# Optimization experiments

Hardware: AMD Instinct MI355X
Metric: run time of the kernel (lower is better)

## Reference

```python
import jax, jax.numpy as jnp
import numpy as np

N_NODES = 50000
N_EDGES = 800000
IN_DIM, HID_DIM, OUT_DIM = 128, 128, 64


def setup_inputs() -> dict:
    key = jax.random.key(0)
    ks = jax.random.split(key, 12)
    x = jax.random.normal(ks[0], (N_NODES, IN_DIM), dtype=jnp.float32)
    src = jax.random.randint(ks[1], (N_EDGES,), 0, N_NODES, dtype=jnp.int32)
    dst = jax.random.randint(ks[2], (N_EDGES,), 0, N_NODES, dtype=jnp.int32)
    def lin(k, fan_in, fan_out):
        s = 1.0 / np.sqrt(fan_in)
        kw, kb = jax.random.split(k)
        W = jax.random.uniform(kw, (fan_in, fan_out), jnp.float32, -s, s)
        b = jax.random.uniform(kb, (fan_out,), jnp.float32, -s, s)
        return W, b
    W1, b1 = lin(ks[3], IN_DIM, HID_DIM)
    W2, b2 = lin(ks[4], HID_DIM, HID_DIM)
    W3, b3 = lin(ks[5], HID_DIM, OUT_DIM)
    Wf, bf = lin(ks[6], OUT_DIM, 1)
    return {"x": x, "src": src, "dst": dst,
            "W1": W1, "b1": b1, "W2": W2, "b2": b2,
            "W3": W3, "b3": b3, "Wf": Wf, "bf": bf}


def reference(x, src, dst, W1, b1, W2, b2, W3, b3, Wf, bf):
    n = x.shape[0]
    # GCN symmetric norm with self-loops: deg = in-degree + 1 (self loop)
    ones = jnp.ones(src.shape[0], x.dtype)
    deg = jax.ops.segment_sum(ones, dst, num_segments=n) + 1.0
    dinv = jax.lax.rsqrt(deg)                       # [N]
    edge_norm = dinv[src] * dinv[dst]               # [E]
    self_norm = dinv * dinv                         # [N], self-loop weight

    def gcn(h, W, b):
        h = h @ W                                   # transform first (PyG order)
        agg = jax.ops.segment_sum(h[src] * edge_norm[:, None], dst, num_segments=n)
        agg = agg + h * self_norm[:, None]          # self-loop contribution
        return agg + b

    h = jax.nn.relu(gcn(x, W1, b1))
    h = jax.nn.relu(gcn(h, W2, b2))
    h = jax.nn.relu(gcn(h, W3, b3))
    return h @ Wf + bf                              # [N, 1] per-node scores
```

## Files before the change

### kernel.cpp

```cpp
#include <hip/hip_runtime.h>
#include <hip/hip_bf16.h>

typedef short bf16x8 __attribute__((ext_vector_type(8)));
typedef float f32x4 __attribute__((ext_vector_type(4)));
typedef _Float16 f16x2 __attribute__((ext_vector_type(2)));

static __device__ __forceinline__ unsigned short f2bf_rne(float f) {
    unsigned int u = __float_as_uint(f);
    u += 0x7fff + ((u >> 16) & 1);
    return (unsigned short)(u >> 16);
}
static __device__ __forceinline__ float bf2f(unsigned short h) {
    return __uint_as_float(((unsigned int)h) << 16);
}

static __device__ __forceinline__ void wsplit_one(const float* W, unsigned short* hi,
                                                  unsigned short* lo, int BN, int idx) {
    int k = idx / BN, n = idx % BN;
    float w = W[idx];
    unsigned short h = f2bf_rne(w);
    unsigned short l = f2bf_rne(w - bf2f(h));
    int CT = BN >> 4;
    int kc = k >> 5, quad = (k >> 3) & 3, j = k & 7;
    int ct = n >> 4, c = n & 15;
    int slot = (((kc * CT + ct) * 4 + quad) * 16 + c) * 8 + j;
    hi[slot] = h;
    lo[slot] = l;
}


template<int BN>
static __device__ __forceinline__ void gemm_body(const float* __restrict__ A,
                        const unsigned short* __restrict__ Whi, const unsigned short* __restrict__ Wlo,
                        _Float16* __restrict__ C, int N, int blk,
                        unsigned short* AhiS, unsigned short* AloS) {
    constexpr int CT = BN / 16;
    const int tid = threadIdx.x;
    const int wave = tid >> 6;
    const int lane = tid & 63;
    const int quad = lane >> 4;
    const int c16 = lane & 15;
    const int row0 = blk * 64;

    f32x4 acc[CT];
    #pragma unroll
    for (int t = 0; t < CT; ++t) acc[t] = (f32x4){0.f, 0.f, 0.f, 0.f};

    for (int kc = 0; kc < 4; ++kc) {
        #pragma unroll
        for (int r = 0; r < 2; ++r) {
            int f4 = tid + r * 256;
            int arow = f4 >> 3;
            int c4 = f4 & 7;
            int grow = row0 + arow;
            float4 v = make_float4(0.f, 0.f, 0.f, 0.f);
            if (grow < N) v = *(const float4*)&A[(size_t)grow * 128 + kc * 32 + c4 * 4];
            unsigned short h0 = f2bf_rne(v.x), h1 = f2bf_rne(v.y), h2 = f2bf_rne(v.z), h3 = f2bf_rne(v.w);
            ushort4 hv = make_ushort4(h0, h1, h2, h3);
            ushort4 lv = make_ushort4(f2bf_rne(v.x - bf2f(h0)), f2bf_rne(v.y - bf2f(h1)),
                                      f2bf_rne(v.z - bf2f(h2)), f2bf_rne(v.w - bf2f(h3)));
            int q = c4 >> 1;
            int joff = (c4 & 1) * 4;
            int base = (q * 64 + arow) * 8 + joff;
            *(ushort4*)&AhiS[base] = hv;
            *(ushort4*)&AloS[base] = lv;
        }
        __syncthreads();

        int abase = (quad * 64 + wave * 16 + c16) * 8;
        bf16x8 ahi = *(const bf16x8*)&AhiS[abase];
        bf16x8 alo = *(const bf16x8*)&AloS[abase];

        #pragma unroll
        for (int ct = 0; ct < CT; ++ct) {
            size_t bslot = ((size_t)(kc * CT + ct) * 64 + lane) * 8;
            bf16x8 bhi = *(const bf16x8*)&Whi[bslot];
            bf16x8 blo = *(const bf16x8*)&Wlo[bslot];
            acc[ct] = __builtin_amdgcn_mfma_f32_16x16x32_bf16(ahi, bhi, acc[ct], 0, 0, 0);
            acc[ct] = __builtin_amdgcn_mfma_f32_16x16x32_bf16(ahi, blo, acc[ct], 0, 0, 0);
            acc[ct] = __builtin_amdgcn_mfma_f32_16x16x32_bf16(alo, bhi, acc[ct], 0, 0, 0);
        }
        __syncthreads();
    }

    #pragma unroll
    for (int ct = 0; ct < CT; ++ct) {
        int col = ct * 16 + c16;
        _Float16* Cq = C + (size_t)(col >> 5) * N * 32 + (col & 31);
        #pragma unroll
        for (int r = 0; r < 4; ++r) {
            int grow = row0 + wave * 16 + quad * 4 + r;
            if (grow < N) Cq[(size_t)grow * 32] = (_Float16)acc[ct][r];
        }
    }
}


__global__ __launch_bounds__(256) void k_count_wsplit(const int* __restrict__ dst, int* __restrict__ deg,
                          int* __restrict__ rank,
                          const float* __restrict__ W1, const float* __restrict__ W2, const float* __restrict__ W3,
                          unsigned short* __restrict__ W1hi, unsigned short* __restrict__ W1lo,
                          unsigned short* __restrict__ W2hi, unsigned short* __restrict__ W2lo,
                          unsigned short* __restrict__ W3hi, unsigned short* __restrict__ W3lo,
                          int E) {
    int e = blockIdx.x * blockDim.x + threadIdx.x;
    if (e < E) rank[e] = atomicAdd(&deg[dst[e]], 1);
    if (e < 128 * 128) {
        wsplit_one(W1, W1hi, W1lo, 128, e);
        wsplit_one(W2, W2hi, W2lo, 128, e);
    }
    if (e < 128 * 64) wsplit_one(W3, W3hi, W3lo, 64, e);
}

__global__ __launch_bounds__(1024) void k_scan(const int* __restrict__ deg, float* __restrict__ dinv,
                                               int* __restrict__ row_start,
                                               float* __restrict__ outp, const float* __restrict__ bf,
                                               int N) {
    __shared__ int s[1024];
    __shared__ int wsum[16];
    __shared__ int prefix;
    const int t = threadIdx.x;
    const int base = blockIdx.x * 1024;

    {
        int v = 0;
        for (int j = t; j < base; j += 1024) v += deg[j];
        for (int off = 32; off > 0; off >>= 1) v += __shfl_down(v, off, 64);
        if ((t & 63) == 0) wsum[t >> 6] = v;
        __syncthreads();
        if (t == 0) {
            int acc = 0;
            #pragma unroll
            for (int k = 0; k < 16; ++k) acc += wsum[k];
            prefix = acc;
        }
    }

    int i = base + t;
    int v = 0;
    if (i < N) {
        v = deg[i];
        dinv[i] = rsqrtf((float)v + 1.0f);
        outp[i] = bf[0];
    }
    s[t] = v;
    __syncthreads();
    for (int off = 1; off < 1024; off <<= 1) {
        int x = (t >= off) ? s[t - off] : 0;
        __syncthreads();
        s[t] += x;
        __syncthreads();
    }
    if (i <= N) row_start[i] = prefix + s[t] - v;
}


__global__ __launch_bounds__(256, 2) void k_gemm1_scatter(const float* __restrict__ A,
                          const unsigned short* __restrict__ Whi, const unsigned short* __restrict__ Wlo,
                          _Float16* __restrict__ C, int N, int gemmGrid,
                          const int* __restrict__ src, const int* __restrict__ dst,
                          const int* __restrict__ row_start, const int* __restrict__ rank,
                          const float* __restrict__ dinv, int2* __restrict__ cv, int E) {
    __shared__ unsigned short AhiS[4 * 64 * 8];
    __shared__ unsigned short AloS[4 * 64 * 8];
    if ((int)blockIdx.x < gemmGrid) {
        gemm_body<128>(A, Whi, Wlo, C, N, blockIdx.x, AhiS, AloS);
    } else {
        int e = (blockIdx.x - gemmGrid) * 256 + threadIdx.x;
        if (e < E) {
            int d = dst[e];
            int s = src[e];
            cv[row_start[d] + rank[e]] = make_int2(s, __float_as_int(dinv[s]));
        }
    }
}

template<int BN>
__global__ __launch_bounds__(256, 2) void k_gemm_mfma(const float* __restrict__ A,
                        const unsigned short* __restrict__ Whi, const unsigned short* __restrict__ Wlo,
                        _Float16* __restrict__ C, int N) {
    __shared__ unsigned short AhiS[4 * 64 * 8];
    __shared__ unsigned short AloS[4 * 64 * 8];
    gemm_body<BN>(A, Whi, Wlo, C, N, blockIdx.x, AhiS, AloS);
}


__global__ __launch_bounds__(256) void k_agg128q(const _Float16* __restrict__ t, float* __restrict__ outp,
                      const int* __restrict__ row_start, const int2* __restrict__ cv,
                      const float* __restrict__ dinv, const float* __restrict__ bias,
                      int N) {
    int q = blockIdx.x / 12500;
    int node = (blockIdx.x - q * 12500) * 4 + (threadIdx.x >> 6);
    int lane = threadIdx.x & 63;
    int l16 = lane & 15;
    int g4 = lane >> 4;
    const f16x2* tp = (const f16x2*)(t + (size_t)q * N * 32);
    int p = row_start[node];
    int end = row_start[node + 1];
    float2 accA = make_float2(0.f, 0.f);
    float2 accB = make_float2(0.f, 0.f);

    while (p < end) {
        int idx = p + lane;
        int2 h = (idx < end) ? cv[idx] : make_int2(0, 0);
        int cnt = min(end - p, 64);
        int rounds = (cnt + 15) >> 4;
        for (int r = 0; r < rounds; ++r) {
            int base = r * 16 + g4 * 4;
            int s0 = __shfl(h.x, base + 0, 64), s1 = __shfl(h.x, base + 1, 64);
            int s2 = __shfl(h.x, base + 2, 64), s3 = __shfl(h.x, base + 3, 64);
            float w0 = __int_as_float(__shfl(h.y, base + 0, 64));
            float w1 = __int_as_float(__shfl(h.y, base + 1, 64));
            float w2 = __int_as_float(__shfl(h.y, base + 2, 64));
            float w3 = __int_as_float(__shfl(h.y, base + 3, 64));
            f16x2 v0 = tp[s0 * 16 + l16];
            f16x2 v1 = tp[s1 * 16 + l16];
            f16x2 v2 = tp[s2 * 16 + l16];
            f16x2 v3 = tp[s3 * 16 + l16];
            accA.x += w0 * (float)v0.x; accA.y += w0 * (float)v0.y;
            accB.x += w1 * (float)v1.x; accB.y += w1 * (float)v1.y;
            accA.x += w2 * (float)v2.x; accA.y += w2 * (float)v2.y;
            accB.x += w3 * (float)v3.x; accB.y += w3 * (float)v3.y;
        }
        p += 64;
    }
    float sx = accA.x + accB.x;
    float sy = accA.y + accB.y;
    sx += __shfl_xor(sx, 16, 64); sx += __shfl_xor(sx, 32, 64);
    sy += __shfl_xor(sy, 16, 64); sy += __shfl_xor(sy, 32, 64);

    float di = dinv[node];
    f16x2 sv = tp[node * 16 + l16];
    float2 bv = ((const float2*)bias)[q * 16 + l16];
    float rx = fmaxf(di * sx + di * di * (float)sv.x + bv.x, 0.f);
    float ry = fmaxf(di * sy + di * di * (float)sv.y + bv.y, 0.f);
    if (lane < 16)
        ((float2*)outp)[(size_t)node * 64 + q * 16 + l16] = make_float2(rx, ry);
}

__global__ __launch_bounds__(256) void k_agg64_final(const _Float16* __restrict__ t, float* __restrict__ outp,
                      const int* __restrict__ row_start, const int2* __restrict__ cv,
                      const float* __restrict__ dinv, const float* __restrict__ bias,
                      const float* __restrict__ Wf,
                      int N) {
    int q = blockIdx.x / 12500;
    int node = (blockIdx.x - q * 12500) * 4 + (threadIdx.x >> 6);
    int lane = threadIdx.x & 63;
    int l16 = lane & 15;
    int g4 = lane >> 4;
    const f16x2* tp = (const f16x2*)(t + (size_t)q * N * 32);
    int p = row_start[node];
    int end = row_start[node + 1];
    float2 accA = make_float2(0.f, 0.f);
    float2 accB = make_float2(0.f, 0.f);

    while (p < end) {
        int idx = p + lane;
        int2 h = (idx < end) ? cv[idx] : make_int2(0, 0);
        int cnt = min(end - p, 64);
        int rounds = (cnt + 15) >> 4;
        for (int r = 0; r < rounds; ++r) {
            int base = r * 16 + g4 * 4;
            int s0 = __shfl(h.x, base + 0, 64), s1 = __shfl(h.x, base + 1, 64);
            int s2 = __shfl(h.x, base + 2, 64), s3 = __shfl(h.x, base + 3, 64);
            float w0 = __int_as_float(__shfl(h.y, base + 0, 64));
            float w1 = __int_as_float(__shfl(h.y, base + 1, 64));
            float w2 = __int_as_float(__shfl(h.y, base + 2, 64));
            float w3 = __int_as_float(__shfl(h.y, base + 3, 64));
            f16x2 v0 = tp[s0 * 16 + l16];
            f16x2 v1 = tp[s1 * 16 + l16];
            f16x2 v2 = tp[s2 * 16 + l16];
            f16x2 v3 = tp[s3 * 16 + l16];
            accA.x += w0 * (float)v0.x; accA.y += w0 * (float)v0.y;
            accB.x += w1 * (float)v1.x; accB.y += w1 * (float)v1.y;
            accA.x += w2 * (float)v2.x; accA.y += w2 * (float)v2.y;
            accB.x += w3 * (float)v3.x; accB.y += w3 * (float)v3.y;
        }
        p += 64;
    }
    float sx = accA.x + accB.x;
    float sy = accA.y + accB.y;
    sx += __shfl_xor(sx, 16, 64); sx += __shfl_xor(sx, 32, 64);
    sy += __shfl_xor(sy, 16, 64); sy += __shfl_xor(sy, 32, 64);

    float di = dinv[node];
    f16x2 sv = tp[node * 16 + l16];
    float2 bv = ((const float2*)bias)[q * 16 + l16];
    float rx = fmaxf(di * sx + di * di * (float)sv.x + bv.x, 0.f);
    float ry = fmaxf(di * sy + di * di * (float)sv.y + bv.y, 0.f);
    float2 wf = ((const float2*)Wf)[q * 16 + l16];
    float partial = rx * wf.x + ry * wf.y;
    partial += __shfl_xor(partial, 1, 64);
    partial += __shfl_xor(partial, 2, 64);
    partial += __shfl_xor(partial, 4, 64);
    partial += __shfl_xor(partial, 8, 64);
    if (lane == 0) atomicAdd(&outp[node], partial);
}


extern "C" void kernel_launch(void* const* d_in, const int* in_sizes, int n_in,
                              void* d_out, int out_size, void* d_ws, size_t ws_size,
                              hipStream_t stream) {
    const float* x  = (const float*)d_in[0];
    const int*   src = (const int*)d_in[1];
    const int*   dst = (const int*)d_in[2];
    const float* W1 = (const float*)d_in[3];
    const float* b1 = (const float*)d_in[4];
    const float* W2 = (const float*)d_in[5];
    const float* b2 = (const float*)d_in[6];
    const float* W3 = (const float*)d_in[7];
    const float* b3 = (const float*)d_in[8];
    const float* Wf = (const float*)d_in[9];
    const float* bf = (const float*)d_in[10];
    float* out = (float*)d_out;

    const int N = 50000;
    const int E = 800000;

    char* ws = (char*)d_ws;
    size_t off = 0;
    auto alloc = [&](size_t bytes) -> void* {
        void* p = (void*)(ws + off);
        off += (bytes + 511) & ~((size_t)511);
        return p;
    };
    int*   deg       = (int*)alloc((size_t)N * 4);
    float* dinv      = (float*)alloc((size_t)N * 4);
    int*   row_start = (int*)alloc((size_t)(N + 1) * 4);
    int*   rank      = (int*)alloc((size_t)E * 4);
    int2*  cv        = (int2*)alloc((size_t)E * 8);
    _Float16* bufT   = (_Float16*)alloc((size_t)N * 128 * 2);
    float* bufH      = (float*)alloc((size_t)N * 128 * 4);
    unsigned short* W1hi = (unsigned short*)alloc(128 * 128 * 2);
    unsigned short* W1lo = (unsigned short*)alloc(128 * 128 * 2);
    unsigned short* W2hi = (unsigned short*)alloc(128 * 128 * 2);
    unsigned short* W2lo = (unsigned short*)alloc(128 * 128 * 2);
    unsigned short* W3hi = (unsigned short*)alloc(128 * 64 * 2);
    unsigned short* W3lo = (unsigned short*)alloc(128 * 64 * 2);

    hipMemsetAsync(deg, 0, (size_t)N * 4, stream);

    k_count_wsplit<<<(E + 255) / 256, 256, 0, stream>>>(dst, deg, rank, W1, W2, W3,
                                                        W1hi, W1lo, W2hi, W2lo, W3hi, W3lo, E);
    int NB = (N + 1023) / 1024;
    k_scan<<<NB, 1024, 0, stream>>>(deg, dinv, row_start, out, bf, N);

    int gemmGrid = (N + 63) / 64;
    int scatGrid = (E + 255) / 256;
    int agg128Grid = N;
    int agg64Grid  = N / 2;

    k_gemm1_scatter<<<gemmGrid + scatGrid, 256, 0, stream>>>(x, W1hi, W1lo, bufT, N, gemmGrid,
                                                             src, dst, row_start, rank, dinv, cv, E);
    k_agg128q<<<agg128Grid, 256, 0, stream>>>(bufT, bufH, row_start, cv, dinv, b1, N);
    k_gemm_mfma<128><<<gemmGrid, 256, 0, stream>>>(bufH, W2hi, W2lo, bufT, N);
    k_agg128q<<<agg128Grid, 256, 0, stream>>>(bufT, bufH, row_start, cv, dinv, b2, N);
    k_gemm_mfma<64><<<gemmGrid, 256, 0, stream>>>(bufH, W3hi, W3lo, bufT, N);
    k_agg64_final<<<agg64Grid, 256, 0, stream>>>(bufT, out, row_start, cv, dinv, b3, Wf, N);
}
```

Measured before the change: 338.6 us.

## Interleave feature-quarter blocks per node group and simplify gather loop

Remaps block indices so that the blocks handling different feature quarters of the same node group are adjacent in launch order, so the shared CSR row data and neighbor indices are reused in cache across quarters. The inner gather loop becomes a single-accumulator loop over 4 edges per step with unroll 4, replacing the manual 4-way unrolled loop with two accumulators. Output stores become nontemporal. This risks a longer dependency chain on one accumulator pair, and it assumes the block count matches the new 8-way interleave.

```diff
diff --git a/kernel.cpp b/kernel.cpp
--- a/kernel.cpp
+++ b/kernel.cpp
@@ -189,53 +189,48 @@
                       const int* __restrict__ row_start, const int2* __restrict__ cv,
                       const float* __restrict__ dinv, const float* __restrict__ bias,
                       int N) {
-    int q = blockIdx.x / 12500;
-    int node = (blockIdx.x - q * 12500) * 4 + (threadIdx.x >> 6);
+    int b = blockIdx.x;
+    int sub = b & 7;
+    int q = sub >> 1;
+    int nb = ((b >> 3) << 1) | (sub & 1);
+    int node = nb * 4 + (threadIdx.x >> 6);
     int lane = threadIdx.x & 63;
     int l16 = lane & 15;
     int g4 = lane >> 4;
-    const f16x2* tp = (const f16x2*)(t + (size_t)q * N * 32);
+    const f16x2* tp = (const f16x2*)(t + (size_t)q * (size_t)N * 32);
     int p = row_start[node];
     int end = row_start[node + 1];
-    float2 accA = make_float2(0.f, 0.f);
-    float2 accB = make_float2(0.f, 0.f);
+    float ax = 0.f, ay = 0.f;
 
     while (p < end) {
         int idx = p + lane;
         int2 h = (idx < end) ? cv[idx] : make_int2(0, 0);
-        int cnt = min(end - p, 64);
-        int rounds = (cnt + 15) >> 4;
-        for (int r = 0; r < rounds; ++r) {
-            int base = r * 16 + g4 * 4;
-            int s0 = __shfl(h.x, base + 0, 64), s1 = __shfl(h.x, base + 1, 64);
-            int s2 = __shfl(h.x, base + 2, 64), s3 = __shfl(h.x, base + 3, 64);
-            float w0 = __int_as_float(__shfl(h.y, base + 0, 64));
-            float w1 = __int_as_float(__shfl(h.y, base + 1, 64));
-            float w2 = __int_as_float(__shfl(h.y, base + 2, 64));
-            float w3 = __int_as_float(__shfl(h.y, base + 3, 64));
-            f16x2 v0 = tp[s0 * 16 + l16];
-            f16x2 v1 = tp[s1 * 16 + l16];
-            f16x2 v2 = tp[s2 * 16 + l16];
-            f16x2 v3 = tp[s3 * 16 + l16];
-            accA.x += w0 * (float)v0.x; accA.y += w0 * (float)v0.y;
-            accB.x += w1 * (float)v1.x; accB.y += w1 * (float)v1.y;
-            accA.x += w2 * (float)v2.x; accA.y += w2 * (float)v2.y;
-            accB.x += w3 * (float)v3.x; accB.y += w3 * (float)v3.y;
+        int cnt = end - p; cnt = cnt > 64 ? 64 : cnt;
+        int jmax = (cnt + 3) >> 2;
+        #pragma unroll 4
+        for (int j = 0; j < jmax; ++j) {
+            int sl = j * 4 + g4;
+            int s = __shfl(h.x, sl, 64);
+            float w = __int_as_float(__shfl(h.y, sl, 64));
+            f16x2 v = tp[(size_t)s * 16 + l16];
+            ax += w * (float)v.x;
+            ay += w * (float)v.y;
         }
         p += 64;
     }
-    float sx = accA.x + accB.x;
-    float sy = accA.y + accB.y;
-    sx += __shfl_xor(sx, 16, 64); sx += __shfl_xor(sx, 32, 64);
-    sy += __shfl_xor(sy, 16, 64); sy += __shfl_xor(sy, 32, 64);
+    ax += __shfl_xor(ax, 16, 64); ax += __shfl_xor(ax, 32, 64);
+    ay += __shfl_xor(ay, 16, 64); ay += __shfl_xor(ay, 32, 64);
 
     float di = dinv[node];
-    f16x2 sv = tp[node * 16 + l16];
+    f16x2 sv = tp[(size_t)node * 16 + l16];
     float2 bv = ((const float2*)bias)[q * 16 + l16];
-    float rx = fmaxf(di * sx + di * di * (float)sv.x + bv.x, 0.f);
-    float ry = fmaxf(di * sy + di * di * (float)sv.y + bv.y, 0.f);
-    if (lane < 16)
-        ((float2*)outp)[(size_t)node * 64 + q * 16 + l16] = make_float2(rx, ry);
+    float rx = fmaxf(di * ax + di * di * (float)sv.x + bv.x, 0.f);
+    float ry = fmaxf(di * ay + di * di * (float)sv.y + bv.y, 0.f);
+    if (g4 == 0) {
+        unsigned long long rv = ((unsigned long long)__float_as_uint(ry) << 32) | __float_as_uint(rx);
+        __builtin_nontemporal_store(rv,
+            (unsigned long long*)&((float2*)outp)[(size_t)node * 64 + q * 16 + l16]);
+    }
 }
 
 __global__ __launch_bounds__(256) void k_agg64_final(const _Float16* __restrict__ t, float* __restrict__ outp,
@@ -243,51 +238,43 @@
                       const float* __restrict__ dinv, const float* __restrict__ bias,
                       const float* __restrict__ Wf,
                       int N) {
-    int q = blockIdx.x / 12500;
-    int node = (blockIdx.x - q * 12500) * 4 + (threadIdx.x >> 6);
+    int b = blockIdx.x;
+    int sub = b & 7;
+    int q = sub >> 2;
+    int hb = ((b >> 3) << 2) | (sub & 3);
+    int node = hb * 4 + (threadIdx.x >> 6);
     int lane = threadIdx.x & 63;
     int l16 = lane & 15;
     int g4 = lane >> 4;
-    const f16x2* tp = (const f16x2*)(t + (size_t)q * N * 32);
+    const f16x2* tp = (const f16x2*)(t + (size_t)q * (size_t)N * 32);
     int p = row_start[node];
     int end = row_start[node + 1];
-    float2 accA = make_float2(0.f, 0.f);
-    float2 accB = make_float2(0.f, 0.f);
+    float ax = 0.f, ay = 0.f;
 
     while (p < end) {
         int idx = p + lane;
         int2 h = (idx < end) ? cv[idx] : make_int2(0, 0);
-        int cnt = min(end - p, 64);
-        int rounds = (cnt + 15) >> 4;
-        for (int r = 0; r < rounds; ++r) {
-            int base = r * 16 + g4 * 4;
-            int s0 = __shfl(h.x, base + 0, 64), s1 = __shfl(h.x, base + 1, 64);
-            int s2 = __shfl(h.x, base + 2, 64), s3 = __shfl(h.x, base + 3, 64);
-            float w0 = __int_as_float(__shfl(h.y, base + 0, 64));
-            float w1 = __int_as_float(__shfl(h.y, base + 1, 64));
-            float w2 = __int_as_float(__shfl(h.y, base + 2, 64));
-            float w3 = __int_as_float(__shfl(h.y, base + 3, 64));
-            f16x2 v0 = tp[s0 * 16 + l16];
-            f16x2 v1 = tp[s1 * 16 + l16];
-            f16x2 v2 = tp[s2 * 16 + l16];
-            f16x2 v3 = tp[s3 * 16 + l16];
-            accA.x += w0 * (float)v0.x; accA.y += w0 * (float)v0.y;
-            accB.x += w1 * (float)v1.x; accB.y += w1 * (float)v1.y;
-            accA.x += w2 * (float)v2.x; accA.y += w2 * (float)v2.y;
-            accB.x += w3 * (float)v3.x; accB.y += w3 * (float)v3.y;
+        int cnt = end - p; cnt = cnt > 64 ? 64 : cnt;
+        int jmax = (cnt + 3) >> 2;
+        #pragma unroll 4
+        for (int j = 0; j < jmax; ++j) {
+            int sl = j * 4 + g4;
+            int s = __shfl(h.x, sl, 64);
+            float w = __int_as_float(__shfl(h.y, sl, 64));
+            f16x2 v = tp[(size_t)s * 16 + l16];
+            ax += w * (float)v.x;
+            ay += w * (float)v.y;
         }
         p += 64;
     }
-    float sx = accA.x + accB.x;
-    float sy = accA.y + accB.y;
-    sx += __shfl_xor(sx, 16, 64); sx += __shfl_xor(sx, 32, 64);
-    sy += __shfl_xor(sy, 16, 64); sy += __shfl_xor(sy, 32, 64);
+    ax += __shfl_xor(ax, 16, 64); ax += __shfl_xor(ax, 32, 64);
+    ay += __shfl_xor(ay, 16, 64); ay += __shfl_xor(ay, 32, 64);
 
     float di = dinv[node];
-    f16x2 sv = tp[node * 16 + l16];
+    f16x2 sv = tp[(size_t)node * 16 + l16];
     float2 bv = ((const float2*)bias)[q * 16 + l16];
-    float rx = fmaxf(di * sx + di * di * (float)sv.x + bv.x, 0.f);
-    float ry = fmaxf(di * sy + di * di * (float)sv.y + bv.y, 0.f);
+    float rx = fmaxf(di * ax + di * di * (float)sv.x + bv.x, 0.f);
+    float ry = fmaxf(di * ay + di * di * (float)sv.y + bv.y, 0.f);
     float2 wf = ((const float2*)Wf)[q * 16 + l16];
     float partial = rx * wf.x + ry * wf.y;
     partial += __shfl_xor(partial, 1, 64);
```

Result: slower. 384.9 us (+13.7%).
